# Kernel tuning notes

Measured on AMD Instinct MI355X. Metric: run time of the kernel, lower is better.

## Reference

```python
import jax, jax.numpy as jnp
import numpy as np

HIDDEN = 2048
INTER = 5632
NCODES = 4096
VEC = 8
TOKENS = 4096


def dequant(codebook, idx, scale):
    # codebook: [NCODES, VEC]; idx: [out, in//VEC] int32; scale: [out]
    out, ncol = idx.shape
    w = codebook[idx].reshape(out, ncol * VEC)  # [out, in]
    return w * scale[:, None]


def setup_inputs() -> dict:
    key = jax.random.key(0)
    ks = jax.random.split(key, 10)
    return {
        "x": jax.random.normal(ks[0], (TOKENS, HIDDEN), dtype=jnp.float32),
        "codebook_gate": jax.random.normal(ks[1], (NCODES, VEC), dtype=jnp.float32),
        "idx_gate": jax.random.randint(ks[2], (INTER, HIDDEN // VEC), 0, NCODES, dtype=jnp.int32),
        "scale_gate": jax.random.uniform(ks[3], (INTER,), dtype=jnp.float32, minval=0.01, maxval=0.05),
        "codebook_up": jax.random.normal(ks[4], (NCODES, VEC), dtype=jnp.float32),
        "idx_up": jax.random.randint(ks[5], (INTER, HIDDEN // VEC), 0, NCODES, dtype=jnp.int32),
        "scale_up": jax.random.uniform(ks[6], (INTER,), dtype=jnp.float32, minval=0.01, maxval=0.05),
        "codebook_down": jax.random.normal(ks[7], (NCODES, VEC), dtype=jnp.float32),
        "idx_down": jax.random.randint(ks[8], (HIDDEN, INTER // VEC), 0, NCODES, dtype=jnp.int32),
        "scale_down": jax.random.uniform(ks[9], (HIDDEN,), dtype=jnp.float32, minval=0.01, maxval=0.05),
    }


def reference(x, codebook_gate, idx_gate, scale_gate,
              codebook_up, idx_up, scale_up,
              codebook_down, idx_down, scale_down):
    # Dequantize trellis/codebook weights, then SwiGLU:
    # out = down( silu(gate(x)) * up(x) )
    w_gate = dequant(codebook_gate, idx_gate, scale_gate)  # [INTER, HIDDEN]
    w_up = dequant(codebook_up, idx_up, scale_up)          # [INTER, HIDDEN]
    w_down = dequant(codebook_down, idx_down, scale_down)  # [HIDDEN, INTER]
    gate = jax.nn.silu(x @ w_gate.T)                       # [T, INTER]
    up = x @ w_up.T                                        # [T, INTER]
    return (gate * up) @ w_down.T                          # [T, HIDDEN]
```

## Files before the change

kernel.cpp:

```cpp
#include <hip/hip_runtime.h>

#define HIDDEN 2048
#define INTER  5632
#define TOKENS 4096

#define BM 128
#define BN 128
#define BK 64
#define NT2 (INTER / BK)

using bf16x8 = __attribute__((ext_vector_type(8))) __bf16;
using f32x4  = __attribute__((ext_vector_type(4))) float;

__device__ __forceinline__ unsigned short f2bf(float f) {
    unsigned int u = __float_as_uint(f);
    u += 0x7FFFu + ((u >> 16) & 1u);
    return (unsigned short)(u >> 16);
}

#define GLDS(gptr, lptr) \
    __builtin_amdgcn_global_load_lds((__attribute__((address_space(1))) void*)(gptr), \
                                     (__attribute__((address_space(3))) void*)(lptr), 16, 0, 0)

__global__ __launch_bounds__(512) void prep_kernel(
        const float* __restrict__ x, unsigned short* __restrict__ xb,
        const int* __restrict__ ig, const float* __restrict__ cbg,
        const float* __restrict__ sg, unsigned short* __restrict__ wg,
        const int* __restrict__ iu, const float* __restrict__ cbu,
        const float* __restrict__ su, unsigned short* __restrict__ wu,
        const int* __restrict__ idn, const float* __restrict__ cbd,
        const float* __restrict__ sd, unsigned short* __restrict__ wd) {
    __shared__ unsigned short cbl[4096 * 8];
    const int b = blockIdx.x;
    const int tid = threadIdx.x;

    if (b >= 528) {
        int t = (b - 528) * 512 + tid;
        const float4* x4 = (const float4*)x;
        float4 a = x4[2 * t];
        float4 c = x4[2 * t + 1];
        uint4 o;
        o.x = f2bf(a.x) | ((unsigned int)f2bf(a.y) << 16);
        o.y = f2bf(a.z) | ((unsigned int)f2bf(a.w) << 16);
        o.z = f2bf(c.x) | ((unsigned int)f2bf(c.y) << 16);
        o.w = f2bf(c.z) | ((unsigned int)f2bf(c.w) << 16);
        ((uint4*)xb)[t] = o;
        return;
    }

    const int mat = b / 176;
    const int bl  = b % 176;
    const int* idx; const float* cb; const float* scale; unsigned short* w; int ncol8;
    if (mat == 0)      { idx = ig;  cb = cbg; scale = sg; w = wg; ncol8 = HIDDEN / 8; }
    else if (mat == 1) { idx = iu;  cb = cbu; scale = su; w = wu; ncol8 = HIDDEN / 8; }
    else               { idx = idn; cb = cbd; scale = sd; w = wd; ncol8 = INTER / 8; }

#pragma unroll
    for (int i = 0; i < 8; ++i) {
        int r = i * 512 + tid;
        const float4* c4 = (const float4*)(cb + ((size_t)r << 3));
        float4 a = c4[0];
        float4 c = c4[1];
        uint4 o;
        o.x = f2bf(a.x) | ((unsigned int)f2bf(a.y) << 16);
        o.y = f2bf(a.z) | ((unsigned int)f2bf(a.w) << 16);
        o.z = f2bf(c.x) | ((unsigned int)f2bf(c.y) << 16);
        o.w = f2bf(c.z) | ((unsigned int)f2bf(c.w) << 16);
        ((uint4*)cbl)[r] = o;
    }
    __syncthreads();

    const size_t base = (size_t)bl * 8192;
#pragma unroll 2
    for (int i = 0; i < 16; ++i) {
        size_t t = base + i * 512 + tid;
        int id = idx[t];
        float s = scale[t / ncol8];
        const unsigned short* cw = cbl + ((unsigned)id << 3);
        uint4 cv = *(const uint4*)cw;
        unsigned int ww[4];
#pragma unroll
        for (int j = 0; j < 4; ++j) {
            unsigned int pair = (&cv.x)[j];
            float lo = __uint_as_float(pair << 16) * s;
            float hi = __uint_as_float(pair & 0xFFFF0000u) * s;
            ww[j] = f2bf(lo) | ((unsigned int)f2bf(hi) << 16);
        }
        uint4 o = {ww[0], ww[1], ww[2], ww[3]};
        ((uint4*)w)[t] = o;
    }
}

__device__ __forceinline__ void decode_block(int bid, int nblocks_m, int nblocks_n,
                                             int gN, int* mb, int* nb) {
    int gw = nblocks_m * gN;
    int group = bid / gw;
    int inb = bid % gw;
    int gn = group * gN;
    int width = (nblocks_n - gn < gN) ? (nblocks_n - gn) : gN;
    *mb = inb / width;
    *nb = gn + inb % width;
}

__global__ __launch_bounds__(256, 2) void gemm1_kernel(const unsigned short* __restrict__ X,
                                                       const unsigned short* __restrict__ Wg,
                                                       const unsigned short* __restrict__ Wu,
                                                       unsigned short* __restrict__ H,
                                                       int bid_off) {
    __shared__ unsigned short As[BM * BK];
    __shared__ unsigned short Bgs[BN * BK];
    __shared__ unsigned short Bus[BN * BK];

    const int tid  = threadIdx.x;
    const int lane = tid & 63;
    const int wave = tid >> 6;
    int mb, nb;
    decode_block(blockIdx.x + bid_off, TOKENS / BM, INTER / BN, 4, &mb, &nb);
    const int m0 = mb * BM;
    const int n0 = nb * BN;

    const int srow = tid >> 3;
    const int scol = (tid & 7) << 3;
    const int gcol = (((tid & 7) ^ (srow & 7))) << 3;

    const int wr = wave >> 1;
    const int wc = wave & 1;
    const int ln15 = lane & 15;
    const int lq = lane >> 4;
    const int swr = ln15 & 7;

    f32x4 accg[4][4], accu[4][4];
    const f32x4 z = {0.f, 0.f, 0.f, 0.f};
    for (int i = 0; i < 4; ++i)
        for (int j = 0; j < 4; ++j) { accg[i][j] = z; accu[i][j] = z; }

    for (int kt = 0; kt < HIDDEN / BK; ++kt) {
        const int k0 = kt * BK;
        __syncthreads();
#pragma unroll
        for (int i = 0; i < 4; ++i) {
            const int r = i * 32 + srow;
            GLDS(X  + (size_t)(m0 + r) * HIDDEN + k0 + gcol, As  + r * BK + scol);
            GLDS(Wg + (size_t)(n0 + r) * HIDDEN + k0 + gcol, Bgs + r * BK + scol);
            GLDS(Wu + (size_t)(n0 + r) * HIDDEN + k0 + gcol, Bus + r * BK + scol);
        }
        __syncthreads();
#pragma unroll
        for (int ks = 0; ks < 2; ++ks) {
            bf16x8 af[4], bg[4], bu[4];
            const int pofs = (((ks * 4 + lq) ^ swr)) << 3;
#pragma unroll
            for (int im = 0; im < 4; ++im)
                af[im] = *(const bf16x8*)(As + (wr * 64 + im * 16 + ln15) * BK + pofs);
#pragma unroll
            for (int in = 0; in < 4; ++in) {
                bg[in] = *(const bf16x8*)(Bgs + (wc * 64 + in * 16 + ln15) * BK + pofs);
                bu[in] = *(const bf16x8*)(Bus + (wc * 64 + in * 16 + ln15) * BK + pofs);
            }
#pragma unroll
            for (int im = 0; im < 4; ++im)
#pragma unroll
                for (int in = 0; in < 4; ++in) {
                    accg[im][in] = __builtin_amdgcn_mfma_f32_16x16x32_bf16(af[im], bg[in], accg[im][in], 0, 0, 0);
                    accu[im][in] = __builtin_amdgcn_mfma_f32_16x16x32_bf16(af[im], bu[in], accu[im][in], 0, 0, 0);
                }
        }
    }

#pragma unroll
    for (int im = 0; im < 4; ++im)
#pragma unroll
        for (int in = 0; in < 4; ++in) {
            const int row = m0 + wr * 64 + im * 16 + lq * 4;
            const int col = n0 + wc * 64 + in * 16 + ln15;
#pragma unroll
            for (int r = 0; r < 4; ++r) {
                float g = accg[im][in][r];
                float u = accu[im][in][r];
                float h = g * (1.0f / (1.0f + __expf(-g))) * u;
                H[(size_t)(row + r) * INTER + col] = f2bf(h);
            }
        }
}

__global__ __launch_bounds__(256, 2) void gemm2_kernel(const unsigned short* __restrict__ Hin,
                                                       const unsigned short* __restrict__ Wd,
                                                       float* __restrict__ Out) {
    __shared__ unsigned short As[2][BM * BK];
    __shared__ unsigned short Bs[2][BN * BK];

    const int tid  = threadIdx.x;
    const int lane = tid & 63;
    const int wave = tid >> 6;
    int mb, nb;
    decode_block(blockIdx.x, TOKENS / BM, HIDDEN / BN, 2, &mb, &nb);
    const int m0 = mb * BM;
    const int n0 = nb * BN;

    const int srow = tid >> 3;
    const int scol = (tid & 7) << 3;
    const int gcol = (((tid & 7) ^ (srow & 7))) << 3;

    const int wr = wave >> 1;
    const int wc = wave & 1;
    const int ln15 = lane & 15;
    const int lq = lane >> 4;
    const int swr = ln15 & 7;

    f32x4 acc[4][4];
    const f32x4 z = {0.f, 0.f, 0.f, 0.f};
    for (int i = 0; i < 4; ++i)
        for (int j = 0; j < 4; ++j) acc[i][j] = z;

#define STAGE2(buf, kt) do {                                                        \
        const int k0_ = (kt) * BK;                                                  \
        _Pragma("unroll")                                                           \
        for (int i_ = 0; i_ < 4; ++i_) {                                            \
            const int r_ = i_ * 32 + srow;                                          \
            GLDS(Hin + (size_t)(m0 + r_) * INTER + k0_ + gcol,                      \
                 &As[buf][r_ * BK + scol]);                                         \
        }                                                                           \
        _Pragma("unroll")                                                           \
        for (int i_ = 0; i_ < 4; ++i_) {                                            \
            const int r_ = i_ * 32 + srow;                                          \
            GLDS(Wd + (size_t)(n0 + r_) * INTER + k0_ + gcol,                       \
                 &Bs[buf][r_ * BK + scol]);                                         \
        }                                                                           \
    } while (0)

    STAGE2(0, 0);
    STAGE2(1, 1);

    for (int t = 0; t < NT2; ++t) {
        const int cur = t & 1;
        if (t + 1 < NT2) {
            asm volatile("s_waitcnt vmcnt(8)" ::: "memory");
        } else {
            asm volatile("s_waitcnt vmcnt(0)" ::: "memory");
        }
        __builtin_amdgcn_s_barrier();

        bf16x8 a0[4], b0[4];
        {
            const int pofs = ((lq ^ swr)) << 3;
#pragma unroll
            for (int im = 0; im < 4; ++im)
                a0[im] = *(const bf16x8*)(&As[cur][(wr * 64 + im * 16 + ln15) * BK + pofs]);
#pragma unroll
            for (int in = 0; in < 4; ++in)
                b0[in] = *(const bf16x8*)(&Bs[cur][(wc * 64 + in * 16 + ln15) * BK + pofs]);
        }
#pragma unroll
        for (int im = 0; im < 4; ++im)
#pragma unroll
            for (int in = 0; in < 4; ++in)
                acc[im][in] = __builtin_amdgcn_mfma_f32_16x16x32_bf16(a0[im], b0[in], acc[im][in], 0, 0, 0);

        bf16x8 a1[4], b1[4];
        {
            const int pofs = (((4 + lq) ^ swr)) << 3;
#pragma unroll
            for (int im = 0; im < 4; ++im)
                a1[im] = *(const bf16x8*)(&As[cur][(wr * 64 + im * 16 + ln15) * BK + pofs]);
#pragma unroll
            for (int in = 0; in < 4; ++in)
                b1[in] = *(const bf16x8*)(&Bs[cur][(wc * 64 + in * 16 + ln15) * BK + pofs]);
        }
        asm volatile("s_waitcnt lgkmcnt(0)" ::: "memory");
        __builtin_amdgcn_s_barrier();
        if (t + 2 < NT2) STAGE2(cur, t + 2);
#pragma unroll
        for (int im = 0; im < 4; ++im)
#pragma unroll
            for (int in = 0; in < 4; ++in)
                acc[im][in] = __builtin_amdgcn_mfma_f32_16x16x32_bf16(a1[im], b1[in], acc[im][in], 0, 0, 0);
    }
#undef STAGE2

#pragma unroll
    for (int im = 0; im < 4; ++im)
#pragma unroll
        for (int in = 0; in < 4; ++in) {
            const int row = m0 + wr * 64 + im * 16 + lq * 4;
            const int col = n0 + wc * 64 + in * 16 + ln15;
#pragma unroll
            for (int r = 0; r < 4; ++r)
                Out[(size_t)(row + r) * HIDDEN + col] = acc[im][in][r];
        }
}

extern "C" void kernel_launch(void* const* d_in, const int* in_sizes, int n_in,
                              void* d_out, int out_size, void* d_ws, size_t ws_size,
                              hipStream_t stream) {
    (void)in_sizes; (void)n_in; (void)out_size; (void)ws_size;

    const float* x   = (const float*)d_in[0];
    const float* cbg = (const float*)d_in[1];
    const int*   ig  = (const int*)d_in[2];
    const float* sg  = (const float*)d_in[3];
    const float* cbu = (const float*)d_in[4];
    const int*   iu  = (const int*)d_in[5];
    const float* su  = (const float*)d_in[6];
    const float* cbd = (const float*)d_in[7];
    const int*   idn = (const int*)d_in[8];
    const float* sd  = (const float*)d_in[9];
    float* out = (float*)d_out;

    char* p = (char*)d_ws;
    unsigned short* Xb = (unsigned short*)p; p += (size_t)TOKENS * HIDDEN * 2;
    unsigned short* Wg = (unsigned short*)p; p += (size_t)INTER * HIDDEN * 2;
    unsigned short* Wu = (unsigned short*)p; p += (size_t)INTER * HIDDEN * 2;
    unsigned short* Wd = (unsigned short*)p; p += (size_t)HIDDEN * INTER * 2;
    unsigned short* H  = (unsigned short*)p; p += (size_t)TOKENS * INTER * 2;

    prep_kernel<<<dim3(528 + 2048), dim3(512), 0, stream>>>(
        x, Xb, ig, cbg, sg, Wg, iu, cbu, su, Wu, idn, cbd, sd, Wd);

    const int g1_blocks = (TOKENS / BM) * (INTER / BN);
    gemm1_kernel<<<dim3(g1_blocks / 2), dim3(256), 0, stream>>>(Xb, Wg, Wu, H, 0);
    gemm1_kernel<<<dim3(g1_blocks / 2), dim3(256), 0, stream>>>(Xb, Wg, Wu, H, g1_blocks / 2);

    gemm2_kernel<<<dim3((TOKENS / BM) * (HIDDEN / BN)), dim3(256), 0, stream>>>(H, Wd, out);
}
```

Measured before the change: 409.3 us.

## Gather codebook from global memory in dequant and merge split gemm1 launches

The dequant blocks no longer stage a bf16 codebook in 64 KB of LDS. Each block now handles 4096 codes and reads fp32 codebook rows directly from global memory, relying on cache hits, with the index and scale loads batched ahead of the gathers. This removes the per-block LDS fill and barrier and the occupancy limit from the large shared array, but adds uncached-looking gathers. The two half-size gemm1 launches are also merged into one launch, which removes a kernel boundary.

After: 377.6 us. 1.08x faster.

```diff
diff --git a/kernel.cpp b/kernel.cpp
--- a/kernel.cpp
+++ b/kernel.cpp
@@ -8,6 +8,11 @@
 #define BN 128
 #define BK 64
 #define NT2 (INTER / BK)
+
+#define DQB 352
+#define DQ_BLOCKS (3 * DQB)
+#define CAST_BLOCKS 2048
+#define CODES_PER_BLOCK 4096
 
 using bf16x8 = __attribute__((ext_vector_type(8))) __bf16;
 using f32x4  = __attribute__((ext_vector_type(4))) float;
@@ -30,12 +35,11 @@
         const float* __restrict__ su, unsigned short* __restrict__ wu,
         const int* __restrict__ idn, const float* __restrict__ cbd,
         const float* __restrict__ sd, unsigned short* __restrict__ wd) {
-    __shared__ unsigned short cbl[4096 * 8];
     const int b = blockIdx.x;
     const int tid = threadIdx.x;
 
-    if (b >= 528) {
-        int t = (b - 528) * 512 + tid;
+    if (b >= DQ_BLOCKS) {
+        int t = (b - DQ_BLOCKS) * 512 + tid;
         const float4* x4 = (const float4*)x;
         float4 a = x4[2 * t];
         float4 c = x4[2 * t + 1];
@@ -48,45 +52,35 @@
         return;
     }
 
-    const int mat = b / 176;
-    const int bl  = b % 176;
+    const int mat = b / DQB;
+    const int bl  = b % DQB;
     const int* idx; const float* cb; const float* scale; unsigned short* w; int ncol8;
     if (mat == 0)      { idx = ig;  cb = cbg; scale = sg; w = wg; ncol8 = HIDDEN / 8; }
     else if (mat == 1) { idx = iu;  cb = cbu; scale = su; w = wu; ncol8 = HIDDEN / 8; }
     else               { idx = idn; cb = cbd; scale = sd; w = wd; ncol8 = INTER / 8; }
 
-#pragma unroll
-    for (int i = 0; i < 8; ++i) {
-        int r = i * 512 + tid;
-        const float4* c4 = (const float4*)(cb + ((size_t)r << 3));
-        float4 a = c4[0];
-        float4 c = c4[1];
+    const size_t base = (size_t)bl * CODES_PER_BLOCK;
+    const float4* cb4 = (const float4*)cb;
+
+    int   ids[8];
+    float ss[8];
+#pragma unroll
+    for (int j = 0; j < 8; ++j) {
+        size_t t = base + j * 512 + tid;
+        ids[j] = idx[t];
+        ss[j]  = scale[t / ncol8];
+    }
+#pragma unroll
+    for (int j = 0; j < 8; ++j) {
+        size_t t = base + j * 512 + tid;
+        float4 c0 = cb4[(size_t)ids[j] * 2];
+        float4 c1 = cb4[(size_t)ids[j] * 2 + 1];
+        float s = ss[j];
         uint4 o;
-        o.x = f2bf(a.x) | ((unsigned int)f2bf(a.y) << 16);
-        o.y = f2bf(a.z) | ((unsigned int)f2bf(a.w) << 16);
-        o.z = f2bf(c.x) | ((unsigned int)f2bf(c.y) << 16);
-        o.w = f2bf(c.z) | ((unsigned int)f2bf(c.w) << 16);
-        ((uint4*)cbl)[r] = o;
-    }
-    __syncthreads();
-
-    const size_t base = (size_t)bl * 8192;
-#pragma unroll 2
-    for (int i = 0; i < 16; ++i) {
-        size_t t = base + i * 512 + tid;
-        int id = idx[t];
-        float s = scale[t / ncol8];
-        const unsigned short* cw = cbl + ((unsigned)id << 3);
-        uint4 cv = *(const uint4*)cw;
-        unsigned int ww[4];
-#pragma unroll
-        for (int j = 0; j < 4; ++j) {
-            unsigned int pair = (&cv.x)[j];
-            float lo = __uint_as_float(pair << 16) * s;
-            float hi = __uint_as_float(pair & 0xFFFF0000u) * s;
-            ww[j] = f2bf(lo) | ((unsigned int)f2bf(hi) << 16);
-        }
-        uint4 o = {ww[0], ww[1], ww[2], ww[3]};
+        o.x = f2bf(c0.x * s) | ((unsigned int)f2bf(c0.y * s) << 16);
+        o.y = f2bf(c0.z * s) | ((unsigned int)f2bf(c0.w * s) << 16);
+        o.z = f2bf(c1.x * s) | ((unsigned int)f2bf(c1.y * s) << 16);
+        o.w = f2bf(c1.z * s) | ((unsigned int)f2bf(c1.w * s) << 16);
         ((uint4*)w)[t] = o;
     }
 }
@@ -105,8 +99,7 @@
 __global__ __launch_bounds__(256, 2) void gemm1_kernel(const unsigned short* __restrict__ X,
                                                        const unsigned short* __restrict__ Wg,
                                                        const unsigned short* __restrict__ Wu,
-                                                       unsigned short* __restrict__ H,
-                                                       int bid_off) {
+                                                       unsigned short* __restrict__ H) {
     __shared__ unsigned short As[BM * BK];
     __shared__ unsigned short Bgs[BN * BK];
     __shared__ unsigned short Bus[BN * BK];
@@ -115,7 +108,7 @@
     const int lane = tid & 63;
     const int wave = tid >> 6;
     int mb, nb;
-    decode_block(blockIdx.x + bid_off, TOKENS / BM, INTER / BN, 4, &mb, &nb);
+    decode_block(blockIdx.x, TOKENS / BM, INTER / BN, 4, &mb, &nb);
     const int m0 = mb * BM;
     const int n0 = nb * BN;
 
@@ -313,12 +306,9 @@
     unsigned short* Wd = (unsigned short*)p; p += (size_t)HIDDEN * INTER * 2;
     unsigned short* H  = (unsigned short*)p; p += (size_t)TOKENS * INTER * 2;
 
-    prep_kernel<<<dim3(528 + 2048), dim3(512), 0, stream>>>(
+    prep_kernel<<<dim3(DQ_BLOCKS + CAST_BLOCKS), dim3(512), 0, stream>>>(
         x, Xb, ig, cbg, sg, Wg, iu, cbu, su, Wu, idn, cbd, sd, Wd);
 
-    const int g1_blocks = (TOKENS / BM) * (INTER / BN);
-    gemm1_kernel<<<dim3(g1_blocks / 2), dim3(256), 0, stream>>>(Xb, Wg, Wu, H, 0);
-    gemm1_kernel<<<dim3(g1_blocks / 2), dim3(256), 0, stream>>>(Xb, Wg, Wu, H, g1_blocks / 2);
-
+    gemm1_kernel<<<dim3((TOKENS / BM) * (INTER / BN)), dim3(256), 0, stream>>>(Xb, Wg, Wu, H);
     gemm2_kernel<<<dim3((TOKENS / BM) * (HIDDEN / BN)), dim3(256), 0, stream>>>(H, Wd, out);
 }
```
